# Optimization experiments

Hardware: AMD Instinct MI355X
Metric: run time of the kernel (lower is better)

## Reference

```python
import jax, jax.numpy as jnp
import numpy as np

N_NODES = 50000
N_EDGES = 800000
IN_DIM = 128
HEADS = 4
CH = 16            # hidden_dim per head
HC = HEADS * CH    # 64
N_GRAPHS = 64
NEG_SLOPE = 0.2


def gat_layer(x, edge_index, edge_attr, W, We, att_src, att_dst, att_edge, bias):
    """PyG GATConv (concat=True, edge_dim=1, eval mode: no dropout)."""
    N = x.shape[0]
    src, dst = edge_index[0], edge_index[1]
    xs = (x @ W).reshape(N, HEADS, CH)                         # [N,H,C]
    a_src = jnp.sum(xs * att_src, axis=-1)                     # [N,H]
    a_dst = jnp.sum(xs * att_dst, axis=-1)                     # [N,H]
    e = (edge_attr @ We).reshape(-1, HEADS, CH)                # [E,H,C]
    a_edge = jnp.sum(e * att_edge, axis=-1)                    # [E,H]
    alpha = a_src[src] + a_dst[dst] + a_edge                   # [E,H]
    alpha = jax.nn.leaky_relu(alpha, NEG_SLOPE)
    # segment softmax over incoming edges of each dst node
    seg_max = jax.ops.segment_max(alpha, dst, num_segments=N)  # [N,H]
    ealpha = jnp.exp(alpha - seg_max[dst])
    seg_sum = jax.ops.segment_sum(ealpha, dst, num_segments=N)
    coef = ealpha / seg_sum[dst]                               # [E,H]
    msg = xs[src] * coef[:, :, None]                           # [E,H,C]
    out = jax.ops.segment_sum(msg, dst, num_segments=N)        # [N,H,C]
    return out.reshape(N, HC) + bias


def setup_inputs() -> dict:
    key = jax.random.key(0)
    ks = jax.random.split(key, 20)
    s = 0.1
    inp = {
        "x": jax.random.normal(ks[0], (N_NODES, IN_DIM), dtype=jnp.float32),
        "edge_index": jax.random.randint(ks[1], (2, N_EDGES), 0, N_NODES, dtype=jnp.int32),
        "edge_attr": jax.random.normal(ks[2], (N_EDGES, 1), dtype=jnp.float32),
        "batch": jnp.sort(jax.random.randint(ks[3], (N_NODES,), 0, N_GRAPHS, dtype=jnp.int32)),
        # layer 1 params
        "W1": jax.random.normal(ks[4], (IN_DIM, HC), dtype=jnp.float32) * s,
        "We1": jax.random.normal(ks[5], (1, HC), dtype=jnp.float32) * s,
        "as1": jax.random.normal(ks[6], (HEADS, CH), dtype=jnp.float32) * s,
        "ad1": jax.random.normal(ks[7], (HEADS, CH), dtype=jnp.float32) * s,
        "ae1": jax.random.normal(ks[8], (HEADS, CH), dtype=jnp.float32) * s,
        "b1": jnp.zeros((HC,), dtype=jnp.float32),
        # layer 2 params (input HC)
        "W2": jax.random.normal(ks[9], (HC, HC), dtype=jnp.float32) * s,
        "We2": jax.random.normal(ks[10], (1, HC), dtype=jnp.float32) * s,
        "as2": jax.random.normal(ks[11], (HEADS, CH), dtype=jnp.float32) * s,
        "ad2": jax.random.normal(ks[12], (HEADS, CH), dtype=jnp.float32) * s,
        "ae2": jax.random.normal(ks[13], (HEADS, CH), dtype=jnp.float32) * s,
        "b2": jnp.zeros((HC,), dtype=jnp.float32),
    }
    return inp


def reference(x, edge_index, edge_attr, batch,
              W1, We1, as1, ad1, ae1, b1,
              W2, We2, as2, ad2, ae2, b2):
    h = gat_layer(x, edge_index, edge_attr, W1, We1, as1, ad1, ae1, b1)
    h = jax.nn.relu(h)                                          # dropout = identity (eval)
    h = gat_layer(h, edge_index, edge_attr, W2, We2, as2, ad2, ae2, b2)
    # global mean pool per graph
    sums = jax.ops.segment_sum(h, batch, num_segments=N_GRAPHS)           # [G,HC]
    cnt = jax.ops.segment_sum(jnp.ones((h.shape[0],), h.dtype), batch,
                              num_segments=N_GRAPHS)
    return sums / jnp.maximum(cnt, 1.0)[:, None]
```

## Files before the change

### kernel.cpp

```cpp
#include <hip/hip_runtime.h>
#include <float.h>

#define N_NODES   50000
#define N_EDGES   800000
#define INDIM1    128
#define HC        64
#define N_GRAPHS  64
#define NEG_SLOPE 0.2f
#define CAP       64
#define CSTRIDE   16

#define FGROUPS   521
#define FTBLK     (3 * FGROUPS)
#define FSBLK     (2 * FGROUPS)
#define FGRID     (5 * FGROUPS + 1)
#define ESTRIDE   (FSBLK * 256)

__global__ __launch_bounds__(256, 4) void fused1_kernel(const float* __restrict__ x,
                                                        const float* __restrict__ W,
                                                        const float* __restrict__ att_s,
                                                        const float* __restrict__ att_d,
                                                        float* __restrict__ xs,
                                                        float* __restrict__ a_src,
                                                        float* __restrict__ a_dst,
                                                        const int* __restrict__ src,
                                                        const int* __restrict__ dst,
                                                        const float* __restrict__ eattr,
                                                        int* __restrict__ cursor,
                                                        int2* __restrict__ csr_se,
                                                        const float* __restrict__ We1,
                                                        const float* __restrict__ ae1,
                                                        const float* __restrict__ We2,
                                                        const float* __restrict__ ae2,
                                                        float* __restrict__ wd) {
    constexpr int K4 = INDIM1 / 4;
    constexpr int NPW = 8;
    __shared__ float4 Wsh[K4 * 64];
    __shared__ float4 xsh[4][2][K4];
    int bid = blockIdx.x;
    int t = threadIdx.x;

    if (bid == FGRID - 1) {
        if (t < 128) {
            const float* We = (t < 64) ? We1 : We2;
            const float* ae = (t < 64) ? ae1 : ae2;
            int l = t & 63;
            float p = We[l] * ae[l];
            for (int off = 1; off < 16; off <<= 1) p += __shfl_xor(p, off);
            if ((l & 15) == 0) wd[(t >> 6) * 4 + (l >> 4)] = p;
        }
        return;
    }

    int grp = bid / 5;
    int rem = bid - grp * 5;
    if (rem >= 3) {
        int sb = grp * 2 + (rem - 3);
        for (int e = sb * 256 + t; e < N_EDGES; e += ESTRIDE) {
            int d = dst[e];
            int c = atomicAdd(&cursor[(size_t)d * CSTRIDE], 1);
            if (c < CAP)
                csr_se[(size_t)d * CAP + c] = make_int2(src[e], __float_as_int(eattr[e]));
        }
        return;
    }

    int tb = grp * 3 + rem;
    for (int i = t; i < K4 * 64; i += 256) {
        int k4 = i >> 6, col = i & 63;
        Wsh[i] = make_float4(W[(4 * k4 + 0) * 64 + col], W[(4 * k4 + 1) * 64 + col],
                             W[(4 * k4 + 2) * 64 + col], W[(4 * k4 + 3) * 64 + col]);
    }
    __syncthreads();
    int w = t >> 6, lane = t & 63;
    float avs = att_s[lane], avd = att_d[lane];
    int node0 = tb * (4 * NPW) + w * NPW;
    for (int ng = 0; ng < NPW; ng += 2) {
        int nbase = node0 + ng;
        if (nbase >= N_NODES) return;
        for (int q = lane; q < 2 * K4; q += 64) {
            int nn = q / K4, kk = q - nn * K4;
            int node = nbase + nn;
            xsh[w][nn][kk] = (node < N_NODES)
                ? ((const float4*)(x + (size_t)node * INDIM1))[kk]
                : make_float4(0.f, 0.f, 0.f, 0.f);
        }
        float acc0 = 0.f, acc1 = 0.f;
#pragma unroll 4
        for (int k4 = 0; k4 < K4; ++k4) {
            float4 wv = Wsh[k4 * 64 + lane];
            float4 x0 = xsh[w][0][k4];
            float4 x1 = xsh[w][1][k4];
            acc0 = fmaf(x0.x, wv.x, acc0);
            acc0 = fmaf(x0.y, wv.y, acc0);
            acc0 = fmaf(x0.z, wv.z, acc0);
            acc0 = fmaf(x0.w, wv.w, acc0);
            acc1 = fmaf(x1.x, wv.x, acc1);
            acc1 = fmaf(x1.y, wv.y, acc1);
            acc1 = fmaf(x1.z, wv.z, acc1);
            acc1 = fmaf(x1.w, wv.w, acc1);
        }
#pragma unroll
        for (int nn = 0; nn < 2; ++nn) {
            int node = nbase + nn;
            if (node >= N_NODES) break;
            float a = nn ? acc1 : acc0;
            xs[(size_t)node * 64 + lane] = a;
            float ps = a * avs;
            float pd = a * avd;
            for (int off = 1; off < 16; off <<= 1) {
                ps += __shfl_xor(ps, off);
                pd += __shfl_xor(pd, off);
            }
            if ((lane & 15) == 0) {
                a_src[node * 4 + (lane >> 4)] = ps;
                a_dst[node * 4 + (lane >> 4)] = pd;
            }
        }
    }
}

template <int INDIM, int NPW>
__global__ __launch_bounds__(256, 4) void transform_kernel(const float* __restrict__ x,
                                                           const float* __restrict__ W,
                                                           const float* __restrict__ att_s,
                                                           const float* __restrict__ att_d,
                                                           float* __restrict__ xs,
                                                           float* __restrict__ a_src,
                                                           float* __restrict__ a_dst) {
    constexpr int K4 = INDIM / 4;
    __shared__ float4 Wsh[K4 * 64];
    __shared__ float4 xsh[4][2][K4];
    int t = threadIdx.x;
    for (int i = t; i < K4 * 64; i += 256) {
        int k4 = i >> 6, col = i & 63;
        Wsh[i] = make_float4(W[(4 * k4 + 0) * 64 + col], W[(4 * k4 + 1) * 64 + col],
                             W[(4 * k4 + 2) * 64 + col], W[(4 * k4 + 3) * 64 + col]);
    }
    __syncthreads();
    int w = t >> 6, lane = t & 63;
    float avs = att_s[lane], avd = att_d[lane];
    int node0 = blockIdx.x * (4 * NPW) + w * NPW;
    for (int ng = 0; ng < NPW; ng += 2) {
        int nbase = node0 + ng;
        if (nbase >= N_NODES) return;
        for (int q = lane; q < 2 * K4; q += 64) {
            int nn = q / K4, kk = q - nn * K4;
            int node = nbase + nn;
            xsh[w][nn][kk] = (node < N_NODES)
                ? ((const float4*)(x + (size_t)node * INDIM))[kk]
                : make_float4(0.f, 0.f, 0.f, 0.f);
        }
        float acc0 = 0.f, acc1 = 0.f;
#pragma unroll 4
        for (int k4 = 0; k4 < K4; ++k4) {
            float4 wv = Wsh[k4 * 64 + lane];
            float4 x0 = xsh[w][0][k4];
            float4 x1 = xsh[w][1][k4];
            acc0 = fmaf(x0.x, wv.x, acc0);
            acc0 = fmaf(x0.y, wv.y, acc0);
            acc0 = fmaf(x0.z, wv.z, acc0);
            acc0 = fmaf(x0.w, wv.w, acc0);
            acc1 = fmaf(x1.x, wv.x, acc1);
            acc1 = fmaf(x1.y, wv.y, acc1);
            acc1 = fmaf(x1.z, wv.z, acc1);
            acc1 = fmaf(x1.w, wv.w, acc1);
        }
#pragma unroll
        for (int nn = 0; nn < 2; ++nn) {
            int node = nbase + nn;
            if (node >= N_NODES) break;
            float a = nn ? acc1 : acc0;
            xs[(size_t)node * 64 + lane] = a;
            float ps = a * avs;
            float pd = a * avd;
            for (int off = 1; off < 16; off <<= 1) {
                ps += __shfl_xor(ps, off);
                pd += __shfl_xor(pd, off);
            }
            if ((lane & 15) == 0) {
                a_src[node * 4 + (lane >> 4)] = ps;
                a_dst[node * 4 + (lane >> 4)] = pd;
            }
        }
    }
}

template <int POOL>
__global__ __launch_bounds__(256, 6) void aggregate_kernel(const float* __restrict__ xs,
                                                           const int2* __restrict__ csr_se,
                                                           const int* __restrict__ degp,
                                                           const float* __restrict__ a_src,
                                                           const float* __restrict__ a_dst,
                                                           const float* __restrict__ wd,
                                                           const float* __restrict__ bias,
                                                           float* __restrict__ outb,
                                                           int do_relu,
                                                           const int* __restrict__ batch,
                                                           float* __restrict__ gout) {
    __shared__ float plds[256];
    int t = threadIdx.x;
    int w = t >> 6, lane = t & 63;
    const int e_idx = lane >> 2;
    const int h4 = lane & 3;
    const int h2 = lane >> 4;
    int nodeA = blockIdx.x * 8 + w * 2;
    int nodeB = nodeA + 1;

    float wdv = wd[h4];
    float bv = bias[lane];
    float advA = a_dst[nodeA * 4 + h4];
    float advB = a_dst[nodeB * 4 + h4];
    int nA = min(degp[(size_t)nodeA * CSTRIDE], CAP);
    int nB = min(degp[(size_t)nodeB * CSTRIDE], CAP);
    int begA = nodeA * CAP, endA = begA + nA;
    int begB = nodeB * CAP, endB = begB + nB;

    float mA = -FLT_MAX, sA = 0.f, accA = 0.f;
    float mB = -FLT_MAX, sB = 0.f, accB = 0.f;

    auto alpha_phase = [&](int beg, int end, int it, float adv,
                           float& m, float& s, float& acc, int& sv, float& wgt) {
        int j = beg + it * 16 + e_idx;
        bool v = j < end;
        sv = 0;
        float a = -FLT_MAX;
        if (v) {
            int2 se = csr_se[j];
            sv = se.x;
            float ea = __int_as_float(se.y);
            float as = a_src[sv * 4 + h4];
            a = as + adv + ea * wdv;
            a = a > 0.f ? a : NEG_SLOPE * a;
        }
        float cm = a;
        cm = fmaxf(cm, __shfl_xor(cm, 4));
        cm = fmaxf(cm, __shfl_xor(cm, 8));
        cm = fmaxf(cm, __shfl_xor(cm, 16));
        cm = fmaxf(cm, __shfl_xor(cm, 32));
        float mn = fmaxf(m, cm);
        float sc = __expf(m - mn);
        wgt = __expf(a - mn);
        s = s * sc + wgt;
        m = mn;
        acc *= __shfl(sc, h2);
    };
    auto gather_phase = [&](int sv, float wgt, float& acc) {
#pragma unroll
        for (int e = 0; e < 16; ++e) {
            int svb = __builtin_amdgcn_readlane(sv, e << 2);
            float wg = __shfl(wgt, (e << 2) | h2);
            acc = fmaf(wg, xs[(size_t)svb * 64 + lane], acc);
        }
    };

    int itA = (nA + 15) >> 4, itB = (nB + 15) >> 4;
    int itC = min(itA, itB);
    for (int it = 0; it < itC; ++it) {
        int svA, svB; float wgtA, wgtB;
        alpha_phase(begA, endA, it, advA, mA, sA, accA, svA, wgtA);
        alpha_phase(begB, endB, it, advB, mB, sB, accB, svB, wgtB);
        gather_phase(svA, wgtA, accA);
        gather_phase(svB, wgtB, accB);
    }
    for (int it = itC; it < itA; ++it) {
        int svA; float wgtA;
        alpha_phase(begA, endA, it, advA, mA, sA, accA, svA, wgtA);
        gather_phase(svA, wgtA, accA);
    }
    for (int it = itC; it < itB; ++it) {
        int svB; float wgtB;
        alpha_phase(begB, endB, it, advB, mB, sB, accB, svB, wgtB);
        gather_phase(svB, wgtB, accB);
    }

    auto finish = [&](float s, float acc) {
        s += __shfl_xor(s, 4);
        s += __shfl_xor(s, 8);
        s += __shfl_xor(s, 16);
        s += __shfl_xor(s, 32);
        float sh = __shfl(s, h2);
        float res = (sh > 0.f) ? acc / sh : 0.f;
        return res + bv;
    };
    float resA = finish(sA, accA);
    float resB = finish(sB, accB);

    if (POOL) {
        int gA = batch[nodeA], gB = batch[nodeB];
        int gF = batch[blockIdx.x * 8];
        int gL = batch[blockIdx.x * 8 + 7];
        if (gF == gL) {
            plds[w * 64 + lane] = resA + resB;
            __syncthreads();
            if (w == 0) {
                float v = plds[lane] + plds[64 + lane] +
                          plds[128 + lane] + plds[192 + lane];
                atomicAdd(&gout[gF * 64 + lane], v);
            }
        } else {
            if (gA == gB) {
                atomicAdd(&gout[gA * 64 + lane], resA + resB);
            } else {
                atomicAdd(&gout[gA * 64 + lane], resA);
                atomicAdd(&gout[gB * 64 + lane], resB);
            }
        }
    } else {
        if (do_relu) { resA = fmaxf(resA, 0.f); resB = fmaxf(resB, 0.f); }
        outb[(size_t)nodeA * 64 + lane] = resA;
        outb[(size_t)nodeB * 64 + lane] = resB;
    }
}

__global__ void pool_div_kernel(float* __restrict__ out, const int* __restrict__ batch) {
    int g = blockIdx.x, t = threadIdx.x;
    int lo = 0, hi = N_NODES;
    while (lo < hi) { int mid = (lo + hi) >> 1; if (batch[mid] < g) lo = mid + 1; else hi = mid; }
    int lo2 = lo, hi2 = N_NODES;
    while (lo2 < hi2) { int mid = (lo2 + hi2) >> 1; if (batch[mid] <= g) lo2 = mid + 1; else hi2 = mid; }
    float c = (float)max(lo2 - lo, 1);
    out[g * 64 + t] /= c;
}


extern "C" void kernel_launch(void* const* d_in, const int* in_sizes, int n_in,
                              void* d_out, int out_size, void* d_ws, size_t ws_size,
                              hipStream_t stream) {
    const float* x    = (const float*)d_in[0];
    const int*   eidx = (const int*)d_in[1];
    const float* eat  = (const float*)d_in[2];
    const int*   batch= (const int*)d_in[3];
    const float* W1   = (const float*)d_in[4];
    const float* We1  = (const float*)d_in[5];
    const float* as1  = (const float*)d_in[6];
    const float* ad1  = (const float*)d_in[7];
    const float* ae1  = (const float*)d_in[8];
    const float* b1   = (const float*)d_in[9];
    const float* W2   = (const float*)d_in[10];
    const float* We2  = (const float*)d_in[11];
    const float* as2  = (const float*)d_in[12];
    const float* ad2  = (const float*)d_in[13];
    const float* ae2  = (const float*)d_in[14];
    const float* b2   = (const float*)d_in[15];
    const int* src  = eidx;
    const int* dstp = eidx + N_EDGES;
    float* out = (float*)d_out;

    char* p = (char*)d_ws;
    auto alloc = [&](size_t bytes) {
        char* r = p;
        p += (bytes + 255) & ~(size_t)255;
        return r;
    };
    int2*  csrse  = (int2*)alloc((size_t)N_NODES * CAP * 8);
    float* xs     = (float*)alloc((size_t)N_NODES * 64 * 4);
    float* hbuf   = (float*)alloc((size_t)N_NODES * 64 * 4);
    float* asrc   = (float*)alloc((size_t)N_NODES * 4 * 4);
    float* adst   = (float*)alloc((size_t)N_NODES * 4 * 4);
    float* wd     = (float*)alloc(64);
    int*   cursor = (int*)alloc((size_t)N_NODES * CSTRIDE * 4);

    hipMemsetAsync(cursor, 0, (size_t)N_NODES * CSTRIDE * 4, stream);
    hipMemsetAsync(d_out, 0, (size_t)N_GRAPHS * 64 * 4, stream);

    const int NPW = 8;
    const int TB = (N_NODES + 4 * NPW - 1) / (4 * NPW);
    const int NB = N_NODES / 8;

    fused1_kernel<<<FGRID, 256, 0, stream>>>(x, W1, as1, ad1, xs, asrc, adst,
                                             src, dstp, eat, cursor, csrse,
                                             We1, ae1, We2, ae2, wd);
    aggregate_kernel<0><<<NB, 256, 0, stream>>>(xs, csrse, cursor, asrc, adst,
                                                wd, b1, hbuf, 1, nullptr, nullptr);
    transform_kernel<HC, NPW><<<TB, 256, 0, stream>>>(hbuf, W2, as2, ad2, xs, asrc, adst);
    aggregate_kernel<1><<<NB, 256, 0, stream>>>(xs, csrse, cursor, asrc, adst,
                                                wd + 4, b2, nullptr, 0, batch, out);
    pool_div_kernel<<<N_GRAPHS, 64, 0, stream>>>(out, batch);
}
```

Measured before the change: 250.5 us.

## Fuse layer-2 linear transform into layer-1 aggregation kernel

```diff
diff --git a/kernel.cpp b/kernel.cpp
--- a/kernel.cpp
+++ b/kernel.cpp
@@ -120,95 +120,36 @@
     }
 }
 
-template <int INDIM, int NPW>
-__global__ __launch_bounds__(256, 4) void transform_kernel(const float* __restrict__ x,
-                                                           const float* __restrict__ W,
-                                                           const float* __restrict__ att_s,
-                                                           const float* __restrict__ att_d,
-                                                           float* __restrict__ xs,
-                                                           float* __restrict__ a_src,
-                                                           float* __restrict__ a_dst) {
-    constexpr int K4 = INDIM / 4;
-    __shared__ float4 Wsh[K4 * 64];
-    __shared__ float4 xsh[4][2][K4];
+__global__ __launch_bounds__(512, 8) void agg1_kernel(const float* __restrict__ xs,
+                                                      const int2* __restrict__ csr_se,
+                                                      const int* __restrict__ degp,
+                                                      const float* __restrict__ a_src,
+                                                      const float* __restrict__ a_dst,
+                                                      const float* __restrict__ wd,
+                                                      const float* __restrict__ bias,
+                                                      const float* __restrict__ W2,
+                                                      const float* __restrict__ as2,
+                                                      const float* __restrict__ ad2,
+                                                      float* __restrict__ xs2,
+                                                      float* __restrict__ asrc2,
+                                                      float* __restrict__ adst2) {
+    __shared__ float W2sh[64 * 64];
+    __shared__ float hshA[8][64];
+    __shared__ float hshB[8][64];
     int t = threadIdx.x;
-    for (int i = t; i < K4 * 64; i += 256) {
-        int k4 = i >> 6, col = i & 63;
-        Wsh[i] = make_float4(W[(4 * k4 + 0) * 64 + col], W[(4 * k4 + 1) * 64 + col],
-                             W[(4 * k4 + 2) * 64 + col], W[(4 * k4 + 3) * 64 + col]);
-    }
-    __syncthreads();
-    int w = t >> 6, lane = t & 63;
-    float avs = att_s[lane], avd = att_d[lane];
-    int node0 = blockIdx.x * (4 * NPW) + w * NPW;
-    for (int ng = 0; ng < NPW; ng += 2) {
-        int nbase = node0 + ng;
-        if (nbase >= N_NODES) return;
-        for (int q = lane; q < 2 * K4; q += 64) {
-            int nn = q / K4, kk = q - nn * K4;
-            int node = nbase + nn;
-            xsh[w][nn][kk] = (node < N_NODES)
-                ? ((const float4*)(x + (size_t)node * INDIM))[kk]
-                : make_float4(0.f, 0.f, 0.f, 0.f);
-        }
-        float acc0 = 0.f, acc1 = 0.f;
-#pragma unroll 4
-        for (int k4 = 0; k4 < K4; ++k4) {
-            float4 wv = Wsh[k4 * 64 + lane];
-            float4 x0 = xsh[w][0][k4];
-            float4 x1 = xsh[w][1][k4];
-            acc0 = fmaf(x0.x, wv.x, acc0);
-            acc0 = fmaf(x0.y, wv.y, acc0);
-            acc0 = fmaf(x0.z, wv.z, acc0);
-            acc0 = fmaf(x0.w, wv.w, acc0);
-            acc1 = fmaf(x1.x, wv.x, acc1);
-            acc1 = fmaf(x1.y, wv.y, acc1);
-            acc1 = fmaf(x1.z, wv.z, acc1);
-            acc1 = fmaf(x1.w, wv.w, acc1);
-        }
-#pragma unroll
-        for (int nn = 0; nn < 2; ++nn) {
-            int node = nbase + nn;
-            if (node >= N_NODES) break;
-            float a = nn ? acc1 : acc0;
-            xs[(size_t)node * 64 + lane] = a;
-            float ps = a * avs;
-            float pd = a * avd;
-            for (int off = 1; off < 16; off <<= 1) {
-                ps += __shfl_xor(ps, off);
-                pd += __shfl_xor(pd, off);
-            }
-            if ((lane & 15) == 0) {
-                a_src[node * 4 + (lane >> 4)] = ps;
-                a_dst[node * 4 + (lane >> 4)] = pd;
-            }
-        }
-    }
-}
-
-template <int POOL>
-__global__ __launch_bounds__(256, 6) void aggregate_kernel(const float* __restrict__ xs,
-                                                           const int2* __restrict__ csr_se,
-                                                           const int* __restrict__ degp,
-                                                           const float* __restrict__ a_src,
-                                                           const float* __restrict__ a_dst,
-                                                           const float* __restrict__ wd,
-                                                           const float* __restrict__ bias,
-                                                           float* __restrict__ outb,
-                                                           int do_relu,
-                                                           const int* __restrict__ batch,
-                                                           float* __restrict__ gout) {
-    __shared__ float plds[256];
-    int t = threadIdx.x;
+    for (int i = t; i < 1024; i += 512)
+        ((float4*)W2sh)[i] = ((const float4*)W2)[i];
+
     int w = t >> 6, lane = t & 63;
     const int e_idx = lane >> 2;
     const int h4 = lane & 3;
     const int h2 = lane >> 4;
-    int nodeA = blockIdx.x * 8 + w * 2;
+    int nodeA = blockIdx.x * 16 + w * 2;
     int nodeB = nodeA + 1;
 
     float wdv = wd[h4];
     float bv = bias[lane];
+    float avs2 = as2[lane], avd2 = ad2[lane];
     float advA = a_dst[nodeA * 4 + h4];
     float advB = a_dst[nodeB * 4 + h4];
     int nA = min(degp[(size_t)nodeA * CSTRIDE], CAP);
@@ -283,33 +224,160 @@
         float res = (sh > 0.f) ? acc / sh : 0.f;
         return res + bv;
     };
+    float hA = fmaxf(finish(sA, accA), 0.f);
+    float hB = fmaxf(finish(sB, accB), 0.f);
+
+    hshA[w][lane] = hA;
+    hshB[w][lane] = hB;
+    __syncthreads();
+
+    float acc2A = 0.f, acc2B = 0.f;
+#pragma unroll
+    for (int k4 = 0; k4 < 16; ++k4) {
+        float4 ha = ((const float4*)hshA[w])[k4];
+        float4 hb = ((const float4*)hshB[w])[k4];
+        float w0 = W2sh[(4 * k4 + 0) * 64 + lane];
+        float w1 = W2sh[(4 * k4 + 1) * 64 + lane];
+        float w2 = W2sh[(4 * k4 + 2) * 64 + lane];
+        float w3 = W2sh[(4 * k4 + 3) * 64 + lane];
+        acc2A = fmaf(ha.x, w0, acc2A); acc2B = fmaf(hb.x, w0, acc2B);
+        acc2A = fmaf(ha.y, w1, acc2A); acc2B = fmaf(hb.y, w1, acc2B);
+        acc2A = fmaf(ha.z, w2, acc2A); acc2B = fmaf(hb.z, w2, acc2B);
+        acc2A = fmaf(ha.w, w3, acc2A); acc2B = fmaf(hb.w, w3, acc2B);
+    }
+    xs2[(size_t)nodeA * 64 + lane] = acc2A;
+    xs2[(size_t)nodeB * 64 + lane] = acc2B;
+    float psA = acc2A * avs2, pdA = acc2A * avd2;
+    float psB = acc2B * avs2, pdB = acc2B * avd2;
+    for (int off = 1; off < 16; off <<= 1) {
+        psA += __shfl_xor(psA, off);
+        pdA += __shfl_xor(pdA, off);
+        psB += __shfl_xor(psB, off);
+        pdB += __shfl_xor(pdB, off);
+    }
+    if ((lane & 15) == 0) {
+        asrc2[nodeA * 4 + (lane >> 4)] = psA;
+        adst2[nodeA * 4 + (lane >> 4)] = pdA;
+        asrc2[nodeB * 4 + (lane >> 4)] = psB;
+        adst2[nodeB * 4 + (lane >> 4)] = pdB;
+    }
+}
+
+__global__ __launch_bounds__(256, 6) void agg2_kernel(const float* __restrict__ xs,
+                                                      const int2* __restrict__ csr_se,
+                                                      const int* __restrict__ degp,
+                                                      const float* __restrict__ a_src,
+                                                      const float* __restrict__ a_dst,
+                                                      const float* __restrict__ wd,
+                                                      const float* __restrict__ bias,
+                                                      const int* __restrict__ batch,
+                                                      float* __restrict__ gout) {
+    __shared__ float plds[256];
+    int t = threadIdx.x;
+    int w = t >> 6, lane = t & 63;
+    const int e_idx = lane >> 2;
+    const int h4 = lane & 3;
+    const int h2 = lane >> 4;
+    int nodeA = blockIdx.x * 8 + w * 2;
+    int nodeB = nodeA + 1;
+
+    float wdv = wd[h4];
+    float bv = bias[lane];
+    float advA = a_dst[nodeA * 4 + h4];
+    float advB = a_dst[nodeB * 4 + h4];
+    int nA = min(degp[(size_t)nodeA * CSTRIDE], CAP);
+    int nB = min(degp[(size_t)nodeB * CSTRIDE], CAP);
+    int begA = nodeA * CAP, endA = begA + nA;
+    int begB = nodeB * CAP, endB = begB + nB;
+
+    float mA = -FLT_MAX, sA = 0.f, accA = 0.f;
+    float mB = -FLT_MAX, sB = 0.f, accB = 0.f;
+
+    auto alpha_phase = [&](int beg, int end, int it, float adv,
+                           float& m, float& s, float& acc, int& sv, float& wgt) {
+        int j = beg + it * 16 + e_idx;
+        bool v = j < end;
+        sv = 0;
+        float a = -FLT_MAX;
+        if (v) {
+            int2 se = csr_se[j];
+            sv = se.x;
+            float ea = __int_as_float(se.y);
+            float as = a_src[sv * 4 + h4];
+            a = as + adv + ea * wdv;
+            a = a > 0.f ? a : NEG_SLOPE * a;
+        }
+        float cm = a;
+        cm = fmaxf(cm, __shfl_xor(cm, 4));
+        cm = fmaxf(cm, __shfl_xor(cm, 8));
+        cm = fmaxf(cm, __shfl_xor(cm, 16));
+        cm = fmaxf(cm, __shfl_xor(cm, 32));
+        float mn = fmaxf(m, cm);
+        float sc = __expf(m - mn);
+        wgt = __expf(a - mn);
+        s = s * sc + wgt;
+        m = mn;
+        acc *= __shfl(sc, h2);
+    };
+    auto gather_phase = [&](int sv, float wgt, float& acc) {
+#pragma unroll
+        for (int e = 0; e < 16; ++e) {
+            int svb = __builtin_amdgcn_readlane(sv, e << 2);
+            float wg = __shfl(wgt, (e << 2) | h2);
+            acc = fmaf(wg, xs[(size_t)svb * 64 + lane], acc);
+        }
+    };
+
+    int itA = (nA + 15) >> 4, itB = (nB + 15) >> 4;
+    int itC = min(itA, itB);
+    for (int it = 0; it < itC; ++it) {
+        int svA, svB; float wgtA, wgtB;
+        alpha_phase(begA, endA, it, advA, mA, sA, accA, svA, wgtA);
+        alpha_phase(begB, endB, it, advB, mB, sB, accB, svB, wgtB);
+        gather_phase(svA, wgtA, accA);
+        gather_phase(svB, wgtB, accB);
+    }
+    for (int it = itC; it < itA; ++it) {
+        int svA; float wgtA;
+        alpha_phase(begA, endA, it, advA, mA, sA, accA, svA, wgtA);
+        gather_phase(svA, wgtA, accA);
+    }
+    for (int it = itC; it < itB; ++it) {
+        int svB; float wgtB;
+        alpha_phase(begB, endB, it, advB, mB, sB, accB, svB, wgtB);
+        gather_phase(svB, wgtB, accB);
+    }
+
+    auto finish = [&](float s, float acc) {
+        s += __shfl_xor(s, 4);
+        s += __shfl_xor(s, 8);
+        s += __shfl_xor(s, 16);
+        s += __shfl_xor(s, 32);
+        float sh = __shfl(s, h2);
+        float res = (sh > 0.f) ? acc / sh : 0.f;
+        return res + bv;
+    };
     float resA = finish(sA, accA);
     float resB = finish(sB, accB);
 
-    if (POOL) {
-        int gA = batch[nodeA], gB = batch[nodeB];
-        int gF = batch[blockIdx.x * 8];
-        int gL = batch[blockIdx.x * 8 + 7];
-        if (gF == gL) {
-            plds[w * 64 + lane] = resA + resB;
-            __syncthreads();
-            if (w == 0) {
-                float v = plds[lane] + plds[64 + lane] +
-                          plds[128 + lane] + plds[192 + lane];
-                atomicAdd(&gout[gF * 64 + lane], v);
-            }
+    int gA = batch[nodeA], gB = batch[nodeB];
+    int gF = batch[blockIdx.x * 8];
+    int gL = batch[blockIdx.x * 8 + 7];
+    if (gF == gL) {
+        plds[w * 64 + lane] = resA + resB;
+        __syncthreads();
+        if (w == 0) {
+            float v = plds[lane] + plds[64 + lane] +
+                      plds[128 + lane] + plds[192 + lane];
+            atomicAdd(&gout[gF * 64 + lane], v);
+        }
+    } else {
+        if (gA == gB) {
+            atomicAdd(&gout[gA * 64 + lane], resA + resB);
         } else {
-            if (gA == gB) {
-                atomicAdd(&gout[gA * 64 + lane], resA + resB);
-            } else {
-                atomicAdd(&gout[gA * 64 + lane], resA);
-                atomicAdd(&gout[gB * 64 + lane], resB);
-            }
-        }
-    } else {
-        if (do_relu) { resA = fmaxf(resA, 0.f); resB = fmaxf(resB, 0.f); }
-        outb[(size_t)nodeA * 64 + lane] = resA;
-        outb[(size_t)nodeB * 64 + lane] = resB;
+            atomicAdd(&gout[gA * 64 + lane], resA);
+            atomicAdd(&gout[gB * 64 + lane], resB);
+        }
     }
 }
 
@@ -358,23 +426,24 @@
     float* hbuf   = (float*)alloc((size_t)N_NODES * 64 * 4);
     float* asrc   = (float*)alloc((size_t)N_NODES * 4 * 4);
     float* adst   = (float*)alloc((size_t)N_NODES * 4 * 4);
+    float* asrc2  = (float*)alloc((size_t)N_NODES * 4 * 4);
+    float* adst2  = (float*)alloc((size_t)N_NODES * 4 * 4);
     float* wd     = (float*)alloc(64);
     int*   cursor = (int*)alloc((size_t)N_NODES * CSTRIDE * 4);
 
     hipMemsetAsync(cursor, 0, (size_t)N_NODES * CSTRIDE * 4, stream);
     hipMemsetAsync(d_out, 0, (size_t)N_GRAPHS * 64 * 4, stream);
 
-    const int NPW = 8;
-    const int TB = (N_NODES + 4 * NPW - 1) / (4 * NPW);
-    const int NB = N_NODES / 8;
+    const int NB1 = N_NODES / 16;
+    const int NB2 = N_NODES / 8;
 
     fused1_kernel<<<FGRID, 256, 0, stream>>>(x, W1, as1, ad1, xs, asrc, adst,
                                              src, dstp, eat, cursor, csrse,
                                              We1, ae1, We2, ae2, wd);
-    aggregate_kernel<0><<<NB, 256, 0, stream>>>(xs, csrse, cursor, asrc, adst,
-                                                wd, b1, hbuf, 1, nullptr, nullptr);
-    transform_kernel<HC, NPW><<<TB, 256, 0, stream>>>(hbuf, W2, as2, ad2, xs, asrc, adst);
-    aggregate_kernel<1><<<NB, 256, 0, stream>>>(xs, csrse, cursor, asrc, adst,
-                                                wd + 4, b2, nullptr, 0, batch, out);
+    agg1_kernel<<<NB1, 512, 0, stream>>>(xs, csrse, cursor, asrc, adst,
+                                         wd, b1, W2, as2, ad2,
+                                         hbuf, asrc2, adst2);
+    agg2_kernel<<<NB2, 256, 0, stream>>>(hbuf, csrse, cursor, asrc2, adst2,
+                                         wd + 4, b2, batch, out);
     pool_div_kernel<<<N_GRAPHS, 64, 0, stream>>>(out, batch);
 }
```

After: 278.3 us. 11.1% more time.
